# Performance work log

Measured on AMD Instinct MI355X. Metric: run time of the kernel, lower is better.

The kernel has to match this reference:

```python
import jax, jax.numpy as jnp
import numpy as np

B, N, M, C = 8, 2048, 2048, 512


def setup_inputs() -> dict:
    key = jax.random.key(0)
    ks = jax.random.split(key, 10)
    s = 1.0 / np.sqrt(C)
    dec_embed = jax.random.normal(ks[0], (B, N, C), dtype=jnp.float32)
    enc_embed = jax.random.normal(ks[1], (B, M, C), dtype=jnp.float32)
    trans_mat = (jax.random.uniform(ks[2], (B, N, M)) < 0.5).astype(jnp.float32)
    Wv = jax.random.uniform(ks[3], (C, C), minval=-s, maxval=s, dtype=jnp.float32)
    bv = jax.random.uniform(ks[4], (C,), minval=-s, maxval=s, dtype=jnp.float32)
    W1 = jax.random.uniform(ks[5], (C, C), minval=-s, maxval=s, dtype=jnp.float32)
    b1 = jax.random.uniform(ks[6], (C,), minval=-s, maxval=s, dtype=jnp.float32)
    W2 = jax.random.uniform(ks[7], (C, C), minval=-s, maxval=s, dtype=jnp.float32)
    b2 = jax.random.uniform(ks[8], (C,), minval=-s, maxval=s, dtype=jnp.float32)
    return {"dec_embed": dec_embed, "enc_embed": enc_embed, "trans_mat": trans_mat,
            "Wv": Wv, "bv": bv, "W1": W1, "b1": b1, "W2": W2, "b2": b2}


def reference(dec_embed, enc_embed, trans_mat, Wv, bv, W1, b1, W2, b2):
    # scores [B,N,M], elementwise-masked by trans_mat
    attn = jnp.einsum('bnc,bmc->bnm', dec_embed, enc_embed) * trans_mat
    # NONSTANDARD masked softmax: zeros participate in softmax (exp(0)=1 in denom),
    # then positions where attn==0 are re-zeroed.
    sm = jax.nn.softmax(attn, axis=-1)
    attn = jnp.where(attn != 0, sm, jnp.zeros((), attn.dtype))
    v = enc_embed @ Wv + bv                      # [B,M,C]
    v = jnp.tanh(jnp.einsum('bnm,bmc->bnc', attn, v))  # [B,N,C]
    g = dec_embed * v + dec_embed                # tanh-gate + residual
    h = jax.nn.relu(g @ W1 + b1)                 # Mlp fc1 + ReLU (drop=0)
    return h @ W2 + b2                           # Mlp fc2
```

## Files before the change

kernel.cpp:

```cpp
#include <hip/hip_runtime.h>
#include <math.h>

#define Bb 8
#define Nn 2048
#define Mm 2048
#define Cc 512

typedef __attribute__((ext_vector_type(8))) _Float16 hfrag;
typedef __attribute__((ext_vector_type(4))) float f4;
typedef __attribute__((ext_vector_type(4))) _Float16 h4;

__device__ __forceinline__ void gld16(const void* g, void* l) {
    __builtin_amdgcn_global_load_lds(
        (const __attribute__((address_space(1))) void*)g,
        (__attribute__((address_space(3))) void*)l, 16, 0, 0);
}

template<int N> __device__ __forceinline__ void wait_vmcnt() {
    if constexpr (N == 0)      asm volatile("s_waitcnt vmcnt(0)" ::: "memory");
    else if constexpr (N == 3) asm volatile("s_waitcnt vmcnt(3)" ::: "memory");
    else if constexpr (N == 4) asm volatile("s_waitcnt vmcnt(4)" ::: "memory");
    __builtin_amdgcn_sched_barrier(0);
}

__global__ __launch_bounds__(256, 1) void attn_fused(
    const _Float16* __restrict__ Eg,
    const _Float16* __restrict__ Qg,
    const _Float16* __restrict__ Vg,
    const float*    __restrict__ Mg,
    _Float16* __restrict__ Gg)
{
    __shared__ _Float16 EA[2][256 * 32];
    __shared__ _Float16 QB[2][64 * 32];
    __shared__ _Float16 VA[2][512 * 32];
    __shared__ _Float16 PL[64 * 256];
    __shared__ float MXS[4][64];
    __shared__ float LSS[4][64];

    const int id = blockIdx.x;
    const int bz = id & 7;
    const int n0 = (id >> 3) * 64;

    const _Float16* E0 = Eg + (size_t)bz * ((size_t)Mm * Cc);
    const _Float16* Q0 = Qg + (size_t)bz * ((size_t)Nn * Cc) + (size_t)n0 * Cc;
    const _Float16* V0 = Vg + (size_t)bz * ((size_t)Cc * Mm);
    const float*    M0 = Mg + (size_t)bz * ((size_t)Nn * Mm);

    const int tid = threadIdx.x;
    const int wv = tid >> 6, ln = tid & 63;
    const int lcol = ln & 15, quad = ln >> 4;
    const int soff = (quad ^ ((lcol >> 1) & 3)) * 8;
    char* PLb = (char*)PL;

    f4 o[8][4];
    const f4 z4 = {0.f, 0.f, 0.f, 0.f};
    #pragma unroll
    for (int i = 0; i < 8; ++i)
        #pragma unroll
        for (int j = 0; j < 4; ++j) o[i][j] = z4;
    float mrun[4] = {0.f, 0.f, 0.f, 0.f};
    float lrun[4] = {0.f, 0.f, 0.f, 0.f};

    for (int mt = 0; mt < 8; ++mt) {
        const int m0 = mt * 256;

        f4 sa[4][4];
        #pragma unroll
        for (int i = 0; i < 4; ++i)
            #pragma unroll
            for (int j = 0; j < 4; ++j) sa[i][j] = z4;

        auto SSTAGE = [&](int k0, int p) {
            #pragma unroll
            for (int q = 0; q < 5; ++q) {
                const int c = q * 256 + tid;
                if (c < 1024) {
                    const int r = c >> 2, gsw = (c & 3) ^ ((c >> 3) & 3);
                    gld16(E0 + (size_t)(m0 + r) * Cc + k0 + gsw * 8, &EA[p][c * 8]);
                } else {
                    const int cb = c - 1024;
                    const int r = cb >> 2, gsw = (cb & 3) ^ ((cb >> 3) & 3);
                    gld16(Q0 + (size_t)r * Cc + k0 + gsw * 8, &QB[p][cb * 8]);
                }
            }
        };
        const float* Mkb = M0 + (size_t)(n0 + lcol) * Mm + m0 + wv * 64 + quad * 4;
        f4 mk[4], mkN[4];
        #pragma unroll
        for (int i = 0; i < 4; ++i) mk[i] = *(const f4*)(Mkb + i * 16);

        SSTAGE(0, 0);
        __syncthreads();
        for (int t = 0; t < 16; ++t) {
            const int p = t & 1;
            if (t + 1 < 16) SSTAGE((t + 1) * 32, p ^ 1);
            hfrag af[4], bf[4];
            #pragma unroll
            for (int i = 0; i < 4; ++i)
                af[i] = *(const hfrag*)&EA[p][(wv * 64 + i * 16 + lcol) * 32 + soff];
            #pragma unroll
            for (int j = 0; j < 4; ++j)
                bf[j] = *(const hfrag*)&QB[p][(j * 16 + lcol) * 32 + soff];
            #pragma unroll
            for (int i = 0; i < 4; ++i)
                #pragma unroll
                for (int j = 0; j < 4; ++j)
                    sa[i][j] = __builtin_amdgcn_mfma_f32_16x16x32_f16(af[i], bf[j], sa[i][j], 0, 0, 0);
            if (t + 1 < 16) __syncthreads();
        }

        #pragma unroll
        for (int j = 0; j < 4; ++j) {
            if (j < 3) {
                #pragma unroll
                for (int i = 0; i < 4; ++i)
                    mkN[i] = *(const f4*)(Mkb + (size_t)(j + 1) * 16 * Mm + i * 16);
            }
            #pragma unroll
            for (int i = 0; i < 4; ++i)
                #pragma unroll
                for (int r = 0; r < 4; ++r) sa[i][j][r] *= mk[i][r];
            float mx = 0.f;
            #pragma unroll
            for (int i = 0; i < 4; ++i)
                #pragma unroll
                for (int r = 0; r < 4; ++r) mx = fmaxf(mx, sa[i][j][r]);
            mx = fmaxf(mx, __shfl_xor(mx, 16, 64));
            mx = fmaxf(mx, __shfl_xor(mx, 32, 64));
            if (quad == 0) MXS[wv][j * 16 + lcol] = mx;
            if (j < 3) {
                #pragma unroll
                for (int i = 0; i < 4; ++i) mk[i] = mkN[i];
            }
        }
        __syncthreads();

        float al[4], mnew[4];
        #pragma unroll
        for (int j = 0; j < 4; ++j) {
            const int n = j * 16 + lcol;
            float mm = mrun[j];
            mm = fmaxf(mm, MXS[0][n]); mm = fmaxf(mm, MXS[1][n]);
            mm = fmaxf(mm, MXS[2][n]); mm = fmaxf(mm, MXS[3][n]);
            al[j] = __expf(mrun[j] - mm);
            mrun[j] = mm; mnew[j] = mm;
        }
        #pragma unroll
        for (int j = 0; j < 4; ++j) {
            const int n = j * 16 + lcol;
            float lp = 0.f;
            #pragma unroll
            for (int i = 0; i < 4; ++i) {
                h4 pv;
                #pragma unroll
                for (int r = 0; r < 4; ++r) {
                    const float s = sa[i][j][r];
                    const float e = __expf(s - mnew[j]);
                    lp += e;
                    pv[r] = (s == 0.f) ? (_Float16)0.f : (_Float16)e;
                }
                *(h4*)(PLb + n * 512 +
                       (((wv << 7) + (i << 5) + (quad << 3)) ^ ((n & 7) << 4))) = pv;
            }
            lp += __shfl_xor(lp, 16, 64);
            lp += __shfl_xor(lp, 32, 64);
            if (quad == 0) LSS[wv][n] = lp;
        }
        __syncthreads();

        #pragma unroll
        for (int j = 0; j < 4; ++j) {
            const int n = j * 16 + lcol;
            const float ls = LSS[0][n] + LSS[1][n] + LSS[2][n] + LSS[3][n];
            lrun[j] = lrun[j] * al[j] + ls;
            #pragma unroll
            for (int i = 0; i < 8; ++i)
                #pragma unroll
                for (int r = 0; r < 4; ++r) o[i][j][r] *= al[j];
        }

        auto VSTAGE = [&](int k0, int p) {
            #pragma unroll
            for (int q = 0; q < 8; ++q) {
                const int c = q * 256 + tid;
                const int r = c >> 2, gsw = (c & 3) ^ ((c >> 3) & 3);
                gld16(V0 + (size_t)r * Mm + m0 + k0 + gsw * 8, &VA[p][c * 8]);
            }
        };
        VSTAGE(0, 0);
        __syncthreads();
        for (int t = 0; t < 8; ++t) {
            const int p = t & 1;
            if (t + 1 < 8) VSTAGE((t + 1) * 32, p ^ 1);
            hfrag va[8], pb[4];
            #pragma unroll
            for (int i = 0; i < 8; ++i)
                va[i] = *(const hfrag*)&VA[p][(wv * 128 + i * 16 + lcol) * 32 + soff];
            #pragma unroll
            for (int j = 0; j < 4; ++j) {
                const int n = j * 16 + lcol;
                pb[j] = *(const hfrag*)(PLb + n * 512 +
                        (((t << 6) + (quad << 4)) ^ ((n & 7) << 4)));
            }
            #pragma unroll
            for (int i = 0; i < 8; ++i)
                #pragma unroll
                for (int j = 0; j < 4; ++j)
                    o[i][j] = __builtin_amdgcn_mfma_f32_16x16x32_f16(va[i], pb[j], o[i][j], 0, 0, 0);
            if (t + 1 < 8) __syncthreads();
        }
        __syncthreads();
    }

    const _Float16* Db = Qg + (size_t)bz * ((size_t)Nn * Cc);
    _Float16* Gb = Gg + (size_t)bz * ((size_t)Nn * Cc);
    #pragma unroll
    for (int j = 0; j < 4; ++j) {
        const int n = n0 + j * 16 + lcol;
        const float inv = 1.f / lrun[j];
        #pragma unroll
        for (int i = 0; i < 8; ++i) {
            const int c0 = wv * 128 + i * 16 + quad * 4;
            const h4 dv = *(const h4*)(Db + (size_t)n * Cc + c0);
            h4 gv;
            #pragma unroll
            for (int r = 0; r < 4; ++r) {
                const float a = o[i][j][r] * inv;
                const float th = 1.f - 2.f / (__expf(2.f * a) + 1.f);
                gv[r] = (_Float16)((float)dv[r] * (1.f + th));
            }
            *(h4*)(Gb + (size_t)n * Cc + c0) = gv;
        }
    }
}

template<int EPI, int BN, int SWZ>
__global__ __launch_bounds__(256) void gemm_mfma(
    const _Float16* __restrict__ Ah, long sA, int lda,
    const _Float16* __restrict__ Bh, long sB, int ldb,
    const float* __restrict__ aux, long sAux, int ldaux,
    void* __restrict__ Cout, long sC, int ldc, int K, int GX)
{
    constexpr int NI  = (BN == 128) ? 4 : 2;
    constexpr int ASL = 512;
    constexpr int BSL = BN * 4;
    constexpr int NQ  = (ASL + BSL) / 256;

    __shared__ _Float16 As[3][128 * 32];
    __shared__ _Float16 Bs[3][BN * 32];

    int bx, by, bz;
    if (SWZ == 1) {
        const int id = blockIdx.x;
        bz = id & 7; bx = (id >> 3) % GX; by = (id >> 3) / GX;
    } else if (SWZ == 2) {
        const int id = blockIdx.x;
        bz = 0; bx = (id >> 3) % GX; by = (id & 7) + 8 * ((id >> 3) / GX);
    } else {
        bx = blockIdx.x; by = blockIdx.y; bz = 0;
    }

    const _Float16* A0 = Ah + (size_t)bz * sA;
    const _Float16* B0 = Bh + (size_t)bz * sB;

    const int tid  = threadIdx.x;
    const int wv   = tid >> 6;
    const int ln   = tid & 63;
    const int wx   = (BN == 128) ? (wv & 1) : 0;
    const int wy   = (BN == 128) ? (wv >> 1) : wv;
    const int lcol = ln & 15, quad = ln >> 4;
    const int row0w = wy * (NI * 16);
    const int col0w = wx * 64;

    const int rowBase = by * 128;
    const int colBase = bx * BN;
    const int soff = (quad ^ ((lcol >> 1) & 3)) * 8;

    f4 acc[NI][4];
    const f4 z4 = {0.f, 0.f, 0.f, 0.f};
    #pragma unroll
    for (int i = 0; i < NI; ++i)
        #pragma unroll
        for (int j = 0; j < 4; ++j) acc[i][j] = z4;

    auto STAGE = [&](int k0, int p) {
        #pragma unroll
        for (int q = 0; q < NQ; ++q) {
            const int c = q * 256 + wv * 64 + ln;
            if (c < ASL) {
                const int r = c >> 2;
                const int g = (c & 3) ^ ((c >> 3) & 3);
                gld16(A0 + (size_t)(rowBase + r) * lda + k0 + g * 8, &As[p][c * 8]);
            } else {
                const int cb = c - ASL;
                const int r  = cb >> 2;
                const int g  = (cb & 3) ^ ((cb >> 3) & 3);
                gld16(B0 + (size_t)(colBase + r) * ldb + k0 + g * 8, &Bs[p][cb * 8]);
            }
        }
    };

    const int NT = K >> 5;
    STAGE(0, 0);
    STAGE(32, 1);
    wait_vmcnt<NQ>();
    __builtin_amdgcn_s_barrier();

    int p = 0, pn2 = 2;
    for (int t = 0; t < NT; ++t) {
        if (t + 2 < NT) STAGE((t + 2) * 32, pn2);

        hfrag af[NI], bf_[4];
        #pragma unroll
        for (int i = 0; i < NI; ++i)
            af[i]  = *(const hfrag*)&As[p][(row0w + i * 16 + lcol) * 32 + soff];
        #pragma unroll
        for (int j = 0; j < 4; ++j)
            bf_[j] = *(const hfrag*)&Bs[p][(col0w + j * 16 + lcol) * 32 + soff];

        #pragma unroll
        for (int i = 0; i < NI; ++i)
            #pragma unroll
            for (int j = 0; j < 4; ++j)
                acc[i][j] = __builtin_amdgcn_mfma_f32_16x16x32_f16(af[i], bf_[j], acc[i][j], 0, 0, 0);

        if (t + 1 < NT) {
            if (t + 2 < NT) wait_vmcnt<NQ>();
            else            wait_vmcnt<0>();
            __builtin_amdgcn_s_barrier();
        }
        p   = (p   == 2) ? 0 : p + 1;
        pn2 = (pn2 == 2) ? 0 : pn2 + 1;
    }

    const int crow0 = rowBase + row0w + quad * 4;
    const int ccol0 = colBase + col0w + lcol;

    if (EPI == 1) {
        _Float16* C = (_Float16*)Cout;
        #pragma unroll
        for (int j = 0; j < 4; ++j) {
            const int col = ccol0 + j * 16;
            const float bi = aux[col];
            #pragma unroll
            for (int i = 0; i < NI; ++i) {
                const int rowb = crow0 + i * 16;
                const int bb = rowb >> 11, ml = rowb & 2047;
                h4 st;
                #pragma unroll
                for (int r = 0; r < 4; ++r) st[r] = (_Float16)(acc[i][j][r] + bi);
                *(h4*)(C + (size_t)bb * ((size_t)Cc * Mm) + (size_t)col * Mm + ml) = st;
            }
        }
    } else if (EPI == 3) {
        _Float16* C = (_Float16*)Cout;
        #pragma unroll
        for (int i = 0; i < NI; ++i) {
            const int c0 = crow0 + i * 16;
            const f4 bi = *(const f4*)(aux + c0);
            #pragma unroll
            for (int j = 0; j < 4; ++j) {
                const int n = ccol0 + j * 16;
                h4 hv;
                #pragma unroll
                for (int r = 0; r < 4; ++r)
                    hv[r] = (_Float16)fmaxf(acc[i][j][r] + bi[r], 0.f);
                *(h4*)(C + (size_t)n * ldc + c0) = hv;
            }
        }
    } else {
        float* C = (float*)Cout;
        #pragma unroll
        for (int i = 0; i < NI; ++i) {
            const int c0 = crow0 + i * 16;
            const f4 bi = *(const f4*)(aux + c0);
            #pragma unroll
            for (int j = 0; j < 4; ++j) {
                const int n = ccol0 + j * 16;
                f4 ov;
                #pragma unroll
                for (int r = 0; r < 4; ++r) ov[r] = acc[i][j][r] + bi[r];
                *(f4*)(C + (size_t)n * ldc + c0) = ov;
            }
        }
    }
}

__global__ __launch_bounds__(256) void sconv(const float* __restrict__ x,
                                             _Float16* __restrict__ o)
{
    const size_t i = (size_t)blockIdx.x * 256 + threadIdx.x;
    f4 v = ((const f4*)x)[i];
    h4 hh;
    #pragma unroll
    for (int k = 0; k < 4; ++k) hh[k] = (_Float16)v[k];
    ((h4*)o)[i] = hh;
}

__global__ __launch_bounds__(256) void wconv(const float* s0, const float* s1, const float* s2,
                                             _Float16* d0, _Float16* d1, _Float16* d2)
{
    const float* Sm = blockIdx.z == 0 ? s0 : blockIdx.z == 1 ? s1 : s2;
    _Float16* D = blockIdx.z == 0 ? d0 : blockIdx.z == 1 ? d1 : d2;
    __shared__ float t[32][33];
    const int x = threadIdx.x & 31, y = threadIdx.x >> 5;
    const int gx = blockIdx.x * 32, gy = blockIdx.y * 32;
    #pragma unroll
    for (int yy = y; yy < 32; yy += 8)
        t[yy][x] = Sm[(size_t)(gy + yy) * 512 + gx + x];
    __syncthreads();
    #pragma unroll
    for (int yy = y; yy < 32; yy += 8)
        D[(size_t)(gx + yy) * 512 + gy + x] = (_Float16)t[x][yy];
}

extern "C" void kernel_launch(void* const* d_in, const int* in_sizes, int n_in,
                              void* d_out, int out_size, void* d_ws, size_t ws_size,
                              hipStream_t stream)
{
    const float* dec   = (const float*)d_in[0];
    const float* enc   = (const float*)d_in[1];
    const float* trans = (const float*)d_in[2];
    const float* Wv = (const float*)d_in[3];
    const float* bv = (const float*)d_in[4];
    const float* W1 = (const float*)d_in[5];
    const float* b1 = (const float*)d_in[6];
    const float* W2 = (const float*)d_in[7];
    const float* b2 = (const float*)d_in[8];

    char* ws = (char*)d_ws;
    _Float16* dec_h = (_Float16*)(ws + 0x4600000);
    _Float16* Wvt   = (_Float16*)(ws + 0x5600000);
    _Float16* W1t   = Wvt + 262144;
    _Float16* W2t   = Wvt + 524288;
    _Float16* vT    = (_Float16*)(ws + 0x5800000);
    _Float16* g     = (_Float16*)(ws + 0x6800000);
    _Float16* h     = (_Float16*)(ws + 0x7800000);
    _Float16* enc_h = (_Float16*)d_out;

    sconv<<<dim3(8192), 256, 0, stream>>>(dec, dec_h);
    sconv<<<dim3(8192), 256, 0, stream>>>(enc, enc_h);
    wconv<<<dim3(16, 16, 3), 256, 0, stream>>>(Wv, W1, W2, Wvt, W1t, W2t);

    gemm_mfma<1, 64, 2><<<dim3(1024), 256, 0, stream>>>(
        enc_h, 0, 512, Wvt, 0, 512, bv, 0, 0,
        vT, 0, 0, 512, 8);

    attn_fused<<<dim3(256), 256, 0, stream>>>(enc_h, dec_h, vT, trans, g);

    gemm_mfma<3, 64, 0><<<dim3(256, 4), 256, 0, stream>>>(
        W1t, 0, 512, g, 0, 512, b1, 0, 0,
        h, 0, 512, 512, 0);

    gemm_mfma<4, 64, 0><<<dim3(256, 4), 256, 0, stream>>>(
        W2t, 0, 512, h, 0, 512, b2, 0, 0,
        d_out, 0, 512, 512, 0);
}
```

Baseline: 469.9 us.

## Halve attention query tile and read E/V fragments directly from global

The fused attention kernel now processes 32 query rows per block instead of 64, launching twice as many blocks with a launch bound allowing two blocks per CU. The double-buffered LDS staging of encoder keys, queries and V (global_load_lds plus syncthreads each k-step) is removed; MFMA operands are loaded straight from global memory into registers. The aim is to use more CUs and cut LDS traffic and barriers, at the cost of uncoalesced per-lane global reads, less reuse of E and V per block (each is now read twice as often), and no software prefetch pipelining.

```diff
diff --git a/kernel.cpp b/kernel.cpp
--- a/kernel.cpp
+++ b/kernel.cpp
@@ -23,23 +23,20 @@
     __builtin_amdgcn_sched_barrier(0);
 }
 
-__global__ __launch_bounds__(256, 1) void attn_fused(
+__global__ __launch_bounds__(256, 2) void attn_fused(
     const _Float16* __restrict__ Eg,
     const _Float16* __restrict__ Qg,
     const _Float16* __restrict__ Vg,
     const float*    __restrict__ Mg,
     _Float16* __restrict__ Gg)
 {
-    __shared__ _Float16 EA[2][256 * 32];
-    __shared__ _Float16 QB[2][64 * 32];
-    __shared__ _Float16 VA[2][512 * 32];
-    __shared__ _Float16 PL[64 * 256];
-    __shared__ float MXS[4][64];
-    __shared__ float LSS[4][64];
+    __shared__ _Float16 PL[32 * 256];
+    __shared__ float MXS[4][32];
+    __shared__ float LSS[4][32];
 
     const int id = blockIdx.x;
     const int bz = id & 7;
-    const int n0 = (id >> 3) * 64;
+    const int n0 = (id >> 3) * 32;
 
     const _Float16* E0 = Eg + (size_t)bz * ((size_t)Mm * Cc);
     const _Float16* Q0 = Qg + (size_t)bz * ((size_t)Nn * Cc) + (size_t)n0 * Cc;
@@ -49,73 +46,56 @@
     const int tid = threadIdx.x;
     const int wv = tid >> 6, ln = tid & 63;
     const int lcol = ln & 15, quad = ln >> 4;
-    const int soff = (quad ^ ((lcol >> 1) & 3)) * 8;
     char* PLb = (char*)PL;
 
-    f4 o[8][4];
+    const _Float16* Eln = E0 + (size_t)(wv * 64 + lcol) * Cc + quad * 8;
+    const _Float16* Qln = Q0 + (size_t)lcol * Cc + quad * 8;
+    const _Float16* Vln = V0 + (size_t)(wv * 128 + lcol) * Mm + quad * 8;
+
+    f4 o[8][2];
     const f4 z4 = {0.f, 0.f, 0.f, 0.f};
     #pragma unroll
     for (int i = 0; i < 8; ++i)
         #pragma unroll
-        for (int j = 0; j < 4; ++j) o[i][j] = z4;
-    float mrun[4] = {0.f, 0.f, 0.f, 0.f};
-    float lrun[4] = {0.f, 0.f, 0.f, 0.f};
+        for (int j = 0; j < 2; ++j) o[i][j] = z4;
+    float mrun[2] = {0.f, 0.f};
+    float lrun[2] = {0.f, 0.f};
 
     for (int mt = 0; mt < 8; ++mt) {
         const int m0 = mt * 256;
 
-        f4 sa[4][4];
+        f4 sa[4][2];
         #pragma unroll
         for (int i = 0; i < 4; ++i)
             #pragma unroll
-            for (int j = 0; j < 4; ++j) sa[i][j] = z4;
-
-        auto SSTAGE = [&](int k0, int p) {
-            #pragma unroll
-            for (int q = 0; q < 5; ++q) {
-                const int c = q * 256 + tid;
-                if (c < 1024) {
-                    const int r = c >> 2, gsw = (c & 3) ^ ((c >> 3) & 3);
-                    gld16(E0 + (size_t)(m0 + r) * Cc + k0 + gsw * 8, &EA[p][c * 8]);
-                } else {
-                    const int cb = c - 1024;
-                    const int r = cb >> 2, gsw = (cb & 3) ^ ((cb >> 3) & 3);
-                    gld16(Q0 + (size_t)r * Cc + k0 + gsw * 8, &QB[p][cb * 8]);
-                }
-            }
-        };
+            for (int j = 0; j < 2; ++j) sa[i][j] = z4;
+
+        {
+            const _Float16* Ei0 = Eln + (size_t)m0 * Cc;
+            #pragma unroll
+            for (int t = 0; t < 16; ++t) {
+                hfrag af[4], bf[2];
+                #pragma unroll
+                for (int i = 0; i < 4; ++i)
+                    af[i] = *(const hfrag*)(Ei0 + (size_t)(i * 16) * Cc + t * 32);
+                #pragma unroll
+                for (int j = 0; j < 2; ++j)
+                    bf[j] = *(const hfrag*)(Qln + (size_t)(j * 16) * Cc + t * 32);
+                #pragma unroll
+                for (int i = 0; i < 4; ++i)
+                    #pragma unroll
+                    for (int j = 0; j < 2; ++j)
+                        sa[i][j] = __builtin_amdgcn_mfma_f32_16x16x32_f16(af[i], bf[j], sa[i][j], 0, 0, 0);
+            }
+        }
+
         const float* Mkb = M0 + (size_t)(n0 + lcol) * Mm + m0 + wv * 64 + quad * 4;
-        f4 mk[4], mkN[4];
-        #pragma unroll
-        for (int i = 0; i < 4; ++i) mk[i] = *(const f4*)(Mkb + i * 16);
-
-        SSTAGE(0, 0);
-        __syncthreads();
-        for (int t = 0; t < 16; ++t) {
-            const int p = t & 1;
-            if (t + 1 < 16) SSTAGE((t + 1) * 32, p ^ 1);
-            hfrag af[4], bf[4];
+        #pragma unroll
+        for (int j = 0; j < 2; ++j) {
+            f4 mk[4];
             #pragma unroll
             for (int i = 0; i < 4; ++i)
-                af[i] = *(const hfrag*)&EA[p][(wv * 64 + i * 16 + lcol) * 32 + soff];
-            #pragma unroll
-            for (int j = 0; j < 4; ++j)
-                bf[j] = *(const hfrag*)&QB[p][(j * 16 + lcol) * 32 + soff];
-            #pragma unroll
-            for (int i = 0; i < 4; ++i)
-                #pragma unroll
-                for (int j = 0; j < 4; ++j)
-                    sa[i][j] = __builtin_amdgcn_mfma_f32_16x16x32_f16(af[i], bf[j], sa[i][j], 0, 0, 0);
-            if (t + 1 < 16) __syncthreads();
-        }
-
-        #pragma unroll
-        for (int j = 0; j < 4; ++j) {
-            if (j < 3) {
-                #pragma unroll
-                for (int i = 0; i < 4; ++i)
-                    mkN[i] = *(const f4*)(Mkb + (size_t)(j + 1) * 16 * Mm + i * 16);
-            }
+                mk[i] = *(const f4*)(Mkb + (size_t)j * 16 * Mm + i * 16);
             #pragma unroll
             for (int i = 0; i < 4; ++i)
                 #pragma unroll
@@ -128,16 +108,12 @@
             mx = fmaxf(mx, __shfl_xor(mx, 16, 64));
             mx = fmaxf(mx, __shfl_xor(mx, 32, 64));
             if (quad == 0) MXS[wv][j * 16 + lcol] = mx;
-            if (j < 3) {
-                #pragma unroll
-                for (int i = 0; i < 4; ++i) mk[i] = mkN[i];
-            }
         }
         __syncthreads();
 
-        float al[4], mnew[4];
-        #pragma unroll
-        for (int j = 0; j < 4; ++j) {
+        float al[2], mnew[2];
+        #pragma unroll
+        for (int j = 0; j < 2; ++j) {
             const int n = j * 16 + lcol;
             float mm = mrun[j];
             mm = fmaxf(mm, MXS[0][n]); mm = fmaxf(mm, MXS[1][n]);
@@ -146,7 +122,7 @@
             mrun[j] = mm; mnew[j] = mm;
         }
         #pragma unroll
-        for (int j = 0; j < 4; ++j) {
+        for (int j = 0; j < 2; ++j) {
             const int n = j * 16 + lcol;
             float lp = 0.f;
             #pragma unroll
@@ -169,7 +145,7 @@
         __syncthreads();
 
         #pragma unroll
-        for (int j = 0; j < 4; ++j) {
+        for (int j = 0; j < 2; ++j) {
             const int n = j * 16 + lcol;
             const float ls = LSS[0][n] + LSS[1][n] + LSS[2][n] + LSS[3][n];
             lrun[j] = lrun[j] * al[j] + ls;
@@ -179,25 +155,14 @@
                 for (int r = 0; r < 4; ++r) o[i][j][r] *= al[j];
         }
 
-        auto VSTAGE = [&](int k0, int p) {
-            #pragma unroll
-            for (int q = 0; q < 8; ++q) {
-                const int c = q * 256 + tid;
-                const int r = c >> 2, gsw = (c & 3) ^ ((c >> 3) & 3);
-                gld16(V0 + (size_t)r * Mm + m0 + k0 + gsw * 8, &VA[p][c * 8]);
-            }
-        };
-        VSTAGE(0, 0);
-        __syncthreads();
+        #pragma unroll
         for (int t = 0; t < 8; ++t) {
-            const int p = t & 1;
-            if (t + 1 < 8) VSTAGE((t + 1) * 32, p ^ 1);
-            hfrag va[8], pb[4];
+            hfrag va[8], pb[2];
             #pragma unroll
             for (int i = 0; i < 8; ++i)
-                va[i] = *(const hfrag*)&VA[p][(wv * 128 + i * 16 + lcol) * 32 + soff];
-            #pragma unroll
-            for (int j = 0; j < 4; ++j) {
+                va[i] = *(const hfrag*)(Vln + (size_t)(i * 16) * Mm + m0 + t * 32);
+            #pragma unroll
+            for (int j = 0; j < 2; ++j) {
                 const int n = j * 16 + lcol;
                 pb[j] = *(const hfrag*)(PLb + n * 512 +
                         (((t << 6) + (quad << 4)) ^ ((n & 7) << 4)));
@@ -205,9 +170,8 @@
             #pragma unroll
             for (int i = 0; i < 8; ++i)
                 #pragma unroll
-                for (int j = 0; j < 4; ++j)
+                for (int j = 0; j < 2; ++j)
                     o[i][j] = __builtin_amdgcn_mfma_f32_16x16x32_f16(va[i], pb[j], o[i][j], 0, 0, 0);
-            if (t + 1 < 8) __syncthreads();
         }
         __syncthreads();
     }
@@ -215,7 +179,7 @@
     const _Float16* Db = Qg + (size_t)bz * ((size_t)Nn * Cc);
     _Float16* Gb = Gg + (size_t)bz * ((size_t)Nn * Cc);
     #pragma unroll
-    for (int j = 0; j < 4; ++j) {
+    for (int j = 0; j < 2; ++j) {
         const int n = n0 + j * 16 + lcol;
         const float inv = 1.f / lrun[j];
         #pragma unroll
@@ -446,7 +410,7 @@
         enc_h, 0, 512, Wvt, 0, 512, bv, 0, 0,
         vT, 0, 0, 512, 8);
 
-    attn_fused<<<dim3(256), 256, 0, stream>>>(enc_h, dec_h, vT, trans, g);
+    attn_fused<<<dim3(512), 256, 0, stream>>>(enc_h, dec_h, vT, trans, g);
 
     gemm_mfma<3, 64, 0><<<dim3(256, 4), 256, 0, stream>>>(
         W1t, 0, 512, g, 0, 512, b1, 0, 0,
```

Measured after the change: 591.0 us. +25.8%, slower.
